# Kernel tuning notes

Measured on AMD Instinct MI355X. Metric: run time of the kernel, lower is better.

Reference implementation:

```python
import jax, jax.numpy as jnp
import numpy as np

EPS = 1e-5
NUM_HEADS = 12

def layer_norm(x, g, b):
    mu = jnp.mean(x, axis=-1, keepdims=True)
    var = jnp.var(x, axis=-1, keepdims=True)
    return (x - mu) * jax.lax.rsqrt(var + EPS) * g + b

def setup_inputs() -> dict:
    key = jax.random.key(0)
    ks = jax.random.split(key, 8)
    B, N, Dv, Ds, F = 8, 1024, 768, 512, 768
    def w(k, shape, fan_in):
        return jax.random.normal(k, shape, jnp.float32) * (fan_in ** -0.5)
    return dict(
        visual_features=jax.random.normal(ks[0], (B, N, Dv), jnp.float32),
        semantic_features=jax.random.normal(ks[1], (B, Ds), jnp.float32),
        Wq=w(ks[2], (F, Ds), Ds),
        Wk=w(ks[3], (F, Dv), Dv),
        Wv=w(ks[4], (F, Dv), Dv),
        Wo=w(ks[5], (Dv, F), F),
        bo=jnp.zeros((Dv,), jnp.float32),
        Wg=w(ks[6], (Dv, Dv + Ds), Dv + Ds),
        bg=jnp.zeros((Dv,), jnp.float32),
        gv=jnp.ones((Dv,), jnp.float32),
        bv=jnp.zeros((Dv,), jnp.float32),
        gs=jnp.ones((Ds,), jnp.float32),
        bs=jnp.zeros((Ds,), jnp.float32),
    )

def reference(visual_features, semantic_features, Wq, Wk, Wv, Wo, bo, Wg, bg, gv, bv, gs, bs):
    B, N, Dv = visual_features.shape
    F = Wq.shape[0]
    H = NUM_HEADS
    dh = F // H
    scale = dh ** -0.5
    vis_n = layer_norm(visual_features, gv, bv)           # (B,N,Dv)
    sem_n = layer_norm(semantic_features, gs, bs)         # (B,Ds) — LN over last dim; broadcast-invariant
    # Query is identical for every patch row -> exact single-query collapse of the N x N attention
    q = (sem_n @ Wq.T).reshape(B, H, dh)                  # (B,H,dh)
    k = (vis_n @ Wk.T).reshape(B, N, H, dh).transpose(0, 2, 1, 3)  # (B,H,N,dh)
    v = (vis_n @ Wv.T).reshape(B, N, H, dh).transpose(0, 2, 1, 3)  # (B,H,N,dh)
    scores = jnp.einsum('bhd,bhnd->bhn', q, k) * scale
    attn = jax.nn.softmax(scores, axis=-1)
    ctx = jnp.einsum('bhn,bhnd->bhd', attn, v).reshape(B, F)
    attended = ctx @ Wo.T + bo                            # (B,Dv), same for all N rows (dropout in eval = identity)
    sem_b = jnp.broadcast_to(semantic_features[:, None, :], (B, N, semantic_features.shape[-1]))
    gate_in = jnp.concatenate([visual_features, sem_b], axis=-1)   # (B,N,Dv+Ds)
    gate = jax.nn.sigmoid(gate_in @ Wg.T + bg)            # (B,N,Dv)
    return visual_features + gate * attended[:, None, :]
```

## Files before the change

kernel.cpp:

```cpp
#include <hip/hip_runtime.h>
#include <hip/hip_bf16.h>
#include <math.h>


typedef __attribute__((ext_vector_type(8))) short bf16x8;
typedef __attribute__((ext_vector_type(4))) float f32x4;

#define LN_EPS 1e-5f

__device__ __forceinline__ float bf2f(__hip_bfloat16 h){ return __bfloat162float(h); }

union bfpk8 { uint4 u; __hip_bfloat16 h[8]; };
union bfpk4 { uint2 u; __hip_bfloat16 h[4]; };

__device__ __align__(16) __hip_bfloat16 c_x[8*1024*768];
__device__ __align__(16) __hip_bfloat16 c_sem[8*512];
__device__ __align__(16) __hip_bfloat16 c_Wq[768*512];
__device__ __align__(16) __hip_bfloat16 c_Wk[768*768];
__device__ __align__(16) __hip_bfloat16 c_Wv[768*768];
__device__ __align__(16) __hip_bfloat16 c_Wo[768*768];
__device__ __align__(16) __hip_bfloat16 c_bo[768];
__device__ __align__(16) __hip_bfloat16 c_Wg[768*1280];
__device__ __align__(16) __hip_bfloat16 c_bg[768];
__device__ __align__(16) __hip_bfloat16 c_gv[768];
__device__ __align__(16) __hip_bfloat16 c_bv[768];
__device__ __align__(16) __hip_bfloat16 c_gs[512];
__device__ __align__(16) __hip_bfloat16 c_bs[512];

__device__ __align__(16) __hip_bfloat16 g_gqb[8*16*768];
__device__ __align__(16) float g_A[8*12*768];
__device__ __align__(16) float g_sgq[96];
__device__ __align__(16) float g_bq[96];
__device__ __align__(16) float g_mu[8192];
__device__ __align__(16) float g_rstd[8192];
__device__ __align__(16) float g_w[8*12*1024];
__device__ __align__(16) float g_C[96];
__device__ __align__(16) float g_ctx[8*768];
__device__ __align__(16) float g_att[8*768];

__device__ __forceinline__ int detect_bf16(const void* gv_raw){
    return ((const unsigned int*)gv_raw)[0] == 0x3F803F80u;
}

__device__ __forceinline__ void conv8(const void* __restrict__ src,
                                      __hip_bfloat16* __restrict__ dst,
                                      int g, int isb){
    if(isb){
        ((uint4*)dst)[g] = ((const uint4*)src)[g];
    } else {
        const float* s = (const float*)src + (size_t)g*8;
        bfpk8 o;
        #pragma unroll
        for(int e=0;e<8;e++) o.h[e] = __float2bfloat16(s[e]);
        ((uint4*)dst)[g] = o.u;
    }
}

#define ING_BLKS 1925
__global__ void k_ingest(const void* s1, const void* s2, const void* s3,
                         const void* s4, const void* s5, const void* s6, const void* s7,
                         const void* s8, const void* s9, const void* s10, const void* s11,
                         const void* s12){
    int i = blockIdx.x*256 + threadIdx.x;
    int isb = detect_bf16(s9);
    if     (i <    512) conv8(s1, c_sem, i,         isb);
    else if(i <  49664) conv8(s2, c_Wq,  i-   512,  isb);
    else if(i < 123392) conv8(s3, c_Wk,  i- 49664,  isb);
    else if(i < 197120) conv8(s4, c_Wv,  i-123392,  isb);
    else if(i < 270848) conv8(s5, c_Wo,  i-197120,  isb);
    else if(i < 270944) conv8(s6, c_bo,  i-270848,  isb);
    else if(i < 393824) conv8(s7, c_Wg,  i-270944,  isb);
    else if(i < 393920) conv8(s8, c_bg,  i-393824,  isb);
    else if(i < 394016) conv8(s9, c_gv,  i-393920,  isb);
    else if(i < 394112) conv8(s10,c_bv,  i-394016,  isb);
    else if(i < 394176) conv8(s11,c_gs,  i-394112,  isb);
    else if(i < 394240) conv8(s12,c_bs,  i-394176,  isb);
    else if(i < 467968) g_A[i-394240]   = 0.f;
    else if(i < 468064) g_sgq[i-467968] = 0.f;
    else if(i < 468160) g_bq[i-468064]  = 0.f;
    else if(i < 474304) g_ctx[i-468160] = 0.f;
    else if(i < 480448) g_att[i-474304] = 0.f;
    else if(i < 492736){
        uint4 z; z.x=0; z.y=0; z.z=0; z.w=0;
        ((uint4*)g_gqb)[i-480448] = z;
    }
}

__global__ void k_qhead(){
    __shared__ float s_semn[8*512];
    __shared__ float s_q2[8][64];
    __shared__ float s_sgq[8], s_bq[8];
    const int t = threadIdx.x, h = blockIdx.y;
    {
        int b = t>>5, l = t&31;
        bfpk8 p0, p1;
        p0.u = *(const uint4*)(c_sem + b*512 + l*16);
        p1.u = *(const uint4*)(c_sem + b*512 + l*16 + 8);
        float v[16], s = 0.f, s2 = 0.f;
        #pragma unroll
        for(int e=0;e<8;e++){ v[e]   = bf2f(p0.h[e]); s += v[e];   s2 += v[e]*v[e]; }
        #pragma unroll
        for(int e=0;e<8;e++){ v[8+e] = bf2f(p1.h[e]); s += v[8+e]; s2 += v[8+e]*v[8+e]; }
        #pragma unroll
        for(int o=16;o>0;o>>=1){ s += __shfl_xor(s,o); s2 += __shfl_xor(s2,o); }
        float mu = s*(1.f/512.f);
        float rstd = rsqrtf(s2*(1.f/512.f) - mu*mu + LN_EPS);
        bfpk8 g0, g1, b0, b1;
        g0.u = *(const uint4*)(c_gs + l*16);   g1.u = *(const uint4*)(c_gs + l*16 + 8);
        b0.u = *(const uint4*)(c_bs + l*16);   b1.u = *(const uint4*)(c_bs + l*16 + 8);
        #pragma unroll
        for(int e=0;e<8;e++){
            s_semn[b*512 + l*16 + e]     = (v[e]-mu)*rstd*bf2f(g0.h[e]) + bf2f(b0.h[e]);
            s_semn[b*512 + l*16 + 8 + e] = (v[8+e]-mu)*rstd*bf2f(g1.h[e]) + bf2f(b1.h[e]);
        }
    }
    if(t < 8){ s_sgq[t] = 0.f; s_bq[t] = 0.f; }
    __syncthreads();
    {
        int fi = t & 63, bp = t >> 6;
        int f = h*64 + fi;
        const __hip_bfloat16* wr = c_Wq + (size_t)f*512;
        float a0 = 0.f, a1 = 0.f;
        for(int i0=0;i0<512;i0+=8){
            bfpk8 pk; pk.u = *(const uint4*)(wr + i0);
            #pragma unroll
            for(int c=0;c<8;c++){
                float wv = bf2f(pk.h[c]);
                a0 += wv*s_semn[bp*512 + i0 + c];
                a1 += wv*s_semn[(bp+4)*512 + i0 + c];
            }
        }
        s_q2[bp][fi] = a0; s_q2[bp+4][fi] = a1;
    }
    __syncthreads();
    int dv = blockIdx.x*256 + t;
    float acc[8] = {0,0,0,0,0,0,0,0};
    for(int j=0;j<64;j++){
        float wk = bf2f(c_Wk[(size_t)(h*64+j)*768 + dv]);
        #pragma unroll
        for(int b=0;b<8;b++) acc[b] += s_q2[b][j]*wk;
    }
    float gvv = bf2f(c_gv[dv]), bvv = bf2f(c_bv[dv]);
    #pragma unroll
    for(int b=0;b<8;b++){
        float g = acc[b]*gvv;
        g_gqb[((size_t)b*16+h)*768 + dv] = __float2bfloat16(g);
        float sg = g, sb = bvv*acc[b];
        #pragma unroll
        for(int o=32;o>0;o>>=1){ sg += __shfl_xor(sg,o); sb += __shfl_xor(sb,o); }
        if((t&63)==0){ atomicAdd(&s_sgq[b], sg); atomicAdd(&s_bq[b], sb); }
    }
    __syncthreads();
    if(t < 8){ atomicAdd(&g_sgq[t*12+h], s_sgq[t]); atomicAdd(&g_bq[t*12+h], s_bq[t]); }
}

__global__ __launch_bounds__(64)
void k_scores(const void* __restrict__ xraw, const void* __restrict__ gvraw){
    __shared__ float s_mu[16], s_rstd[16];
    const int b = blockIdx.y;
    const int lane = threadIdx.x;
    const int isb = detect_bf16(gvraw);
    const int fr = lane & 15, quad = lane >> 4;
    const int n_tile = blockIdx.x*16;
    const size_t row = (size_t)b*1024 + n_tile + fr;
    const __hip_bfloat16* Bp = g_gqb + (size_t)b*16*768 + (size_t)fr*768;

    f32x4 acc = {};
    float s = 0.f, s2 = 0.f;
    if(isb){
        const __hip_bfloat16* xr = (const __hip_bfloat16*)xraw + row*768;
        for(int kb=0; kb<768; kb+=32){
            bfpk8 pk; pk.u = *(const uint4*)(xr + kb + quad*8);
            *(uint4*)(c_x + row*768 + kb + quad*8) = pk.u;
            #pragma unroll
            for(int e=0;e<8;e++){ float f = bf2f(pk.h[e]); s += f; s2 += f*f; }
            bf16x8 bfrag = *(const bf16x8*)(Bp + kb + quad*8);
            acc = __builtin_amdgcn_mfma_f32_16x16x32_bf16(*(const bf16x8*)&pk, bfrag, acc, 0,0,0);
        }
    } else {
        const float* xr = (const float*)xraw + row*768;
        for(int kb=0; kb<768; kb+=32){
            f32x4 x0 = *(const f32x4*)(xr + kb + quad*8);
            f32x4 x1 = *(const f32x4*)(xr + kb + quad*8 + 4);
            bfpk8 pk;
            #pragma unroll
            for(int e=0;e<4;e++){ pk.h[e]   = __float2bfloat16(x0[e]); s += x0[e]; s2 += x0[e]*x0[e]; }
            #pragma unroll
            for(int e=0;e<4;e++){ pk.h[4+e] = __float2bfloat16(x1[e]); s += x1[e]; s2 += x1[e]*x1[e]; }
            *(uint4*)(c_x + row*768 + kb + quad*8) = pk.u;
            bf16x8 bfrag = *(const bf16x8*)(Bp + kb + quad*8);
            acc = __builtin_amdgcn_mfma_f32_16x16x32_bf16(*(const bf16x8*)&pk, bfrag, acc, 0,0,0);
        }
    }
    s  += __shfl_xor(s, 16);  s  += __shfl_xor(s, 32);
    s2 += __shfl_xor(s2, 16); s2 += __shfl_xor(s2, 32);
    float mu = s*(1.f/768.f);
    float rstd = rsqrtf(s2*(1.f/768.f) - mu*mu + LN_EPS);
    if(quad == 0){
        g_mu[b*1024 + n_tile + fr] = mu;
        g_rstd[b*1024 + n_tile + fr] = rstd;
        s_mu[fr] = mu; s_rstd[fr] = rstd;
    }
    __syncthreads();
    if(fr < 12){
        float sgqh = g_sgq[b*12+fr];
        float bqh  = g_bq [b*12+fr];
        #pragma unroll
        for(int r=0;r<4;r++){
            int rr = quad*4 + r;
            float val = 0.125f*( s_rstd[rr]*(acc[r] - s_mu[rr]*sgqh) + bqh );
            g_w[((size_t)b*12+fr)*1024 + n_tile + rr] = val;
        }
    }
}

__global__ void k_softmax(){
    int bh = blockIdx.x, b = bh/12, t = threadIdx.x;
    float* sc = g_w + (size_t)bh*1024;
    f32x4 v = *(f32x4*)(sc + t*4);
    float m = fmaxf(fmaxf(v[0],v[1]), fmaxf(v[2],v[3]));
    __shared__ float redm[4], reds[4], redc[4];
    #pragma unroll
    for(int o=32;o>0;o>>=1) m = fmaxf(m, __shfl_xor(m,o));
    if((t&63)==0) redm[t>>6] = m;
    __syncthreads();
    m = fmaxf(fmaxf(redm[0],redm[1]), fmaxf(redm[2],redm[3]));
    float e0=expf(v[0]-m), e1=expf(v[1]-m), e2=expf(v[2]-m), e3=expf(v[3]-m);
    float s = e0+e1+e2+e3;
    #pragma unroll
    for(int o=32;o>0;o>>=1) s += __shfl_xor(s,o);
    if((t&63)==0) reds[t>>6] = s;
    __syncthreads();
    s = reds[0]+reds[1]+reds[2]+reds[3];
    float inv = 1.f/s;
    f32x4 rv = *(f32x4*)(g_rstd + b*1024 + t*4);
    f32x4 mv = *(f32x4*)(g_mu   + b*1024 + t*4);
    f32x4 o4;
    o4[0]=e0*inv*rv[0]; o4[1]=e1*inv*rv[1]; o4[2]=e2*inv*rv[2]; o4[3]=e3*inv*rv[3];
    *(f32x4*)(sc + t*4) = o4;
    float cp = o4[0]*mv[0] + o4[1]*mv[1] + o4[2]*mv[2] + o4[3]*mv[3];
    #pragma unroll
    for(int o=32;o>0;o>>=1) cp += __shfl_xor(cp,o);
    if((t&63)==0) redc[t>>6] = cp;
    __syncthreads();
    if(t==0) g_C[bh] = redc[0]+redc[1]+redc[2]+redc[3];
}

__global__ void k_accA(){
    __shared__ float s_w[12*128];
    int t = threadIdx.x, b = blockIdx.z, n0 = blockIdx.y*128;
    for(int i=t;i<12*128;i+=256){
        int h = i>>7, n = i&127;
        s_w[i] = g_w[((size_t)b*12+h)*1024 + n0 + n];
    }
    __syncthreads();
    int dv = blockIdx.x*256 + t;
    float acc[12] = {0,0,0,0,0,0,0,0,0,0,0,0};
    for(int n=0;n<128;n++){
        float xv = bf2f(c_x[(size_t)(b*1024+n0+n)*768 + dv]);
        #pragma unroll
        for(int h=0;h<12;h++) acc[h] += s_w[h*128+n]*xv;
    }
    #pragma unroll
    for(int h=0;h<12;h++) atomicAdd(&g_A[((size_t)b*12+h)*768 + dv], acc[h]);
}

__global__ void k_ctx(){
    __shared__ float s_wvis[8*260];
    int h = blockIdx.x, ch = blockIdx.y, t = threadIdx.x;
    int base = ch*256;
    for(int i=t;i<8*256;i+=512){
        int b = i>>8, dvl = i&255;
        int dv = base + dvl;
        s_wvis[b*260+dvl] = bf2f(c_gv[dv])*(g_A[((size_t)b*12+h)*768+dv] - g_C[b*12+h]) + bf2f(c_bv[dv]);
    }
    __syncthreads();
    int f = h*64 + (t>>3), b = t&7;
    const __hip_bfloat16* wr = c_Wv + (size_t)f*768 + base;
    float acc = 0.f;
    for(int d0=0;d0<256;d0+=8){
        bfpk8 pk; pk.u = *(const uint4*)(wr + d0);
        #pragma unroll
        for(int c=0;c<8;c++) acc += s_wvis[b*260 + d0 + c]*bf2f(pk.h[c]);
    }
    atomicAdd(&g_ctx[b*768+f], acc);
}

__global__ void k_att(){
    __shared__ float s_ctx[8*260];
    int ch = blockIdx.y, t = threadIdx.x;
    int base = ch*256;
    for(int i=t;i<8*256;i+=512){
        int b = i>>8, fl = i&255;
        s_ctx[b*260+fl] = g_ctx[b*768 + base + fl];
    }
    __syncthreads();
    int dv2 = blockIdx.x*64 + (t>>3), b = t&7;
    const __hip_bfloat16* wr = c_Wo + (size_t)dv2*768 + base;
    float acc = (ch==0) ? bf2f(c_bo[dv2]) : 0.f;
    for(int f0=0;f0<256;f0+=8){
        bfpk8 pk; pk.u = *(const uint4*)(wr + f0);
        #pragma unroll
        for(int c=0;c<8;c++) acc += s_ctx[b*260 + f0 + c]*bf2f(pk.h[c]);
    }
    atomicAdd(&g_att[b*768+dv2], acc);
}

__device__ __forceinline__ void stage_gate(int buf, int kb, int m0, int n0, int b_blk,
                                           __hip_bfloat16* As, __hip_bfloat16* Bs,
                                           int wave, int lane){
    const int rl = lane >> 2;
    const int kc = (lane & 3)*8;
    #pragma unroll
    for(int s=0;s<2;s++){
        int c = wave + 4*s;
        int row = c*16 + rl;
        const __hip_bfloat16* gp = (kb < 768)
            ? c_x + (size_t)(m0+row)*768 + kb + kc
            : c_sem + b_blk*512 + (kb-768) + kc;
        __builtin_amdgcn_global_load_lds(
            (const __attribute__((address_space(1))) void*)gp,
            (__attribute__((address_space(3))) void*)(As + buf*4096 + c*512),
            16, 0, 0);
    }
    {
        int c = wave;
        int row = c*16 + rl;
        const __hip_bfloat16* gp = c_Wg + (size_t)(n0+row)*1280 + kb + kc;
        __builtin_amdgcn_global_load_lds(
            (const __attribute__((address_space(1))) void*)gp,
            (__attribute__((address_space(3))) void*)(Bs + buf*2048 + c*512),
            16, 0, 0);
    }
}

__global__ __launch_bounds__(256)
void k_gate(void* __restrict__ outv, const void* __restrict__ gv_raw){
    __shared__ __align__(16) __hip_bfloat16 As[2*128*32];
    __shared__ __align__(16) __hip_bfloat16 Bs[2*64*32];
    const int isb = detect_bf16(gv_raw);
    const int t = threadIdx.x;
    const int n0 = blockIdx.x*64;
    const int m0 = blockIdx.y*128;
    const int b_blk = m0 >> 10;
    const int lane = t & 63, wave = t >> 6;
    const int wm = (wave>>1)*64, wn = (wave&1)*32;
    const int fr = lane & 15, quad = lane >> 4;

    f32x4 acc[4][2] = {};

    stage_gate(0, 0, m0, n0, b_blk, As, Bs, wave, lane);
    for(int it=0; it<40; it++){
        __syncthreads();
        if(it+1 < 40)
            stage_gate((it+1)&1, (it+1)*32, m0, n0, b_blk, As, Bs, wave, lane);
        const __hip_bfloat16* Ab = As + (it&1)*4096;
        const __hip_bfloat16* Bb = Bs + (it&1)*2048;
        bf16x8 af[4], bfr[2];
        #pragma unroll
        for(int i=0;i<4;i++) af[i]  = *(const bf16x8*)(Ab + (wm + i*16 + fr)*32 + quad*8);
        #pragma unroll
        for(int j=0;j<2;j++) bfr[j] = *(const bf16x8*)(Bb + (wn + j*16 + fr)*32 + quad*8);
        #pragma unroll
        for(int i=0;i<4;i++)
            #pragma unroll
            for(int j=0;j<2;j++)
                acc[i][j] = __builtin_amdgcn_mfma_f32_16x16x32_bf16(af[i], bfr[j], acc[i][j], 0,0,0);
    }

    #pragma unroll
    for(int j=0;j<2;j++){
        int col = n0 + wn + j*16 + fr;
        float attv = g_att[b_blk*768 + col];
        float bgv  = bf2f(c_bg[col]);
        #pragma unroll
        for(int i=0;i<4;i++){
            int mbase = m0 + wm + i*16 + quad*4;
            #pragma unroll
            for(int r=0;r<4;r++){
                int m = mbase + r;
                float g = acc[i][j][r] + bgv;
                g = fminf(fmaxf(g, -60.f), 60.f);
                float gate = 1.f/(1.f + expf(-g));
                float xv = bf2f(c_x[(size_t)m*768 + col]);
                float val = xv + gate*attv;
                size_t idx = (size_t)m*768 + col;
                if(isb) ((__hip_bfloat16*)outv)[idx] = __float2bfloat16(val);
                else    ((float*)outv)[idx] = val;
            }
        }
    }
}

extern "C" void kernel_launch(void* const* d_in, const int* in_sizes, int n_in,
                              void* d_out, int out_size, void* d_ws, size_t ws_size,
                              hipStream_t stream){
    (void)in_sizes; (void)n_in; (void)out_size; (void)d_ws; (void)ws_size;

    k_ingest<<<dim3(ING_BLKS), dim3(256), 0, stream>>>(d_in[1], d_in[2], d_in[3],
                                                       d_in[4], d_in[5], d_in[6], d_in[7],
                                                       d_in[8], d_in[9], d_in[10], d_in[11],
                                                       d_in[12]);
    k_qhead<<<dim3(3,12), dim3(256), 0, stream>>>();
    k_scores<<<dim3(64,8), dim3(64), 0, stream>>>(d_in[0], d_in[9]);
    k_softmax<<<dim3(96), dim3(256), 0, stream>>>();
    k_accA<<<dim3(3,8,8), dim3(256), 0, stream>>>();
    k_ctx<<<dim3(12,3), dim3(512), 0, stream>>>();
    k_att<<<dim3(12,3), dim3(512), 0, stream>>>();
    k_gate<<<dim3(12,64), dim3(256), 0, stream>>>(d_out, d_in[9]);
}
```

Before: 230.9 us.

## Precompute semantic gate term, split-K scores, swizzle LDS and remap gate blocks

The semantic part of the gate GEMM is constant across all N rows of a batch, so it is now computed once per batch in a new small kernel and added as a bias, which shrinks the gate GEMM K from 1280 to 768. The scores kernel now uses four waves per block, each handling a quarter of K, and combines partial MFMA results and LN statistics through shared memory. The gate kernel gains an XOR swizzle on its LDS staging to reduce bank conflicts, plus a block-index remap meant to improve cache locality. These changes add one extra kernel launch and extra shared-memory reductions.

Measured after the change: 210.0 us. 9.1% less time.

```diff
diff --git a/kernel.cpp b/kernel.cpp
--- a/kernel.cpp
+++ b/kernel.cpp
@@ -37,6 +37,7 @@
 __device__ __align__(16) float g_C[96];
 __device__ __align__(16) float g_ctx[8*768];
 __device__ __align__(16) float g_att[8*768];
+__device__ __align__(16) float g_gsem[8*768];
 
 __device__ __forceinline__ int detect_bf16(const void* gv_raw){
     return ((const unsigned int*)gv_raw)[0] == 0x3F803F80u;
@@ -154,22 +155,57 @@
     if(t < 8){ atomicAdd(&g_sgq[t*12+h], s_sgq[t]); atomicAdd(&g_bq[t*12+h], s_bq[t]); }
 }
 
-__global__ __launch_bounds__(64)
+__global__ __launch_bounds__(256)
+void k_gsem(){
+    __shared__ float s_sem[8*512];
+    __shared__ __hip_bfloat16 s_wg[16*520];
+    __shared__ float s_part[128];
+    const int t = threadIdx.x;
+    const int col0 = blockIdx.x*16;
+    for(int i=t;i<512;i+=256){
+        bfpk8 p; p.u = *(const uint4*)(c_sem + i*8);
+        #pragma unroll
+        for(int e=0;e<8;e++) s_sem[i*8+e] = bf2f(p.h[e]);
+    }
+    for(int i=t;i<16*64;i+=256){
+        int rl = i>>6, c = i&63;
+        *(uint4*)(s_wg + rl*520 + c*8) =
+            *(const uint4*)(c_Wg + (size_t)(col0+rl)*1280 + 768 + c*8);
+    }
+    __syncthreads();
+    const int cl = t&15, bh = t>>4, bb = bh&7, half = bh>>3;
+    const __hip_bfloat16* wr = s_wg + cl*520 + half*256;
+    const float* sr = s_sem + bb*512 + half*256;
+    float a = 0.f;
+    for(int k=0;k<256;k+=8){
+        bfpk8 p; p.u = *(const uint4*)(wr + k);
+        #pragma unroll
+        for(int e=0;e<8;e++) a += bf2f(p.h[e])*sr[k+e];
+    }
+    if(half) s_part[t&127] = a;
+    __syncthreads();
+    if(!half) g_gsem[bb*768 + col0 + cl] = a + s_part[t&127];
+}
+
+__global__ __launch_bounds__(256)
 void k_scores(const void* __restrict__ xraw, const void* __restrict__ gvraw){
+    __shared__ float s_acc[256*4];
+    __shared__ float s_s[4][16], s_s2[4][16];
     __shared__ float s_mu[16], s_rstd[16];
     const int b = blockIdx.y;
-    const int lane = threadIdx.x;
+    const int t = threadIdx.x, lane = t & 63, w = t >> 6;
     const int isb = detect_bf16(gvraw);
     const int fr = lane & 15, quad = lane >> 4;
     const int n_tile = blockIdx.x*16;
     const size_t row = (size_t)b*1024 + n_tile + fr;
     const __hip_bfloat16* Bp = g_gqb + (size_t)b*16*768 + (size_t)fr*768;
+    const int k0 = w*192;
 
     f32x4 acc = {};
     float s = 0.f, s2 = 0.f;
     if(isb){
         const __hip_bfloat16* xr = (const __hip_bfloat16*)xraw + row*768;
-        for(int kb=0; kb<768; kb+=32){
+        for(int kb=k0; kb<k0+192; kb+=32){
             bfpk8 pk; pk.u = *(const uint4*)(xr + kb + quad*8);
             *(uint4*)(c_x + row*768 + kb + quad*8) = pk.u;
             #pragma unroll
@@ -179,7 +215,7 @@
         }
     } else {
         const float* xr = (const float*)xraw + row*768;
-        for(int kb=0; kb<768; kb+=32){
+        for(int kb=k0; kb<k0+192; kb+=32){
             f32x4 x0 = *(const f32x4*)(xr + kb + quad*8);
             f32x4 x1 = *(const f32x4*)(xr + kb + quad*8 + 4);
             bfpk8 pk;
@@ -194,15 +230,27 @@
     }
     s  += __shfl_xor(s, 16);  s  += __shfl_xor(s, 32);
     s2 += __shfl_xor(s2, 16); s2 += __shfl_xor(s2, 32);
-    float mu = s*(1.f/768.f);
-    float rstd = rsqrtf(s2*(1.f/768.f) - mu*mu + LN_EPS);
-    if(quad == 0){
-        g_mu[b*1024 + n_tile + fr] = mu;
-        g_rstd[b*1024 + n_tile + fr] = rstd;
-        s_mu[fr] = mu; s_rstd[fr] = rstd;
-    }
-    __syncthreads();
-    if(fr < 12){
+    *(f32x4*)&s_acc[t*4] = acc;
+    if(quad == 0){ s_s[w][fr] = s; s_s2[w][fr] = s2; }
+    __syncthreads();
+    if(w == 0){
+        #pragma unroll
+        for(int ww=1;ww<4;ww++){
+            f32x4 o = *(const f32x4*)&s_acc[(ww*64+lane)*4];
+            acc[0]+=o[0]; acc[1]+=o[1]; acc[2]+=o[2]; acc[3]+=o[3];
+        }
+        if(quad == 0){
+            float st  = s_s[0][fr]+s_s[1][fr]+s_s[2][fr]+s_s[3][fr];
+            float st2 = s_s2[0][fr]+s_s2[1][fr]+s_s2[2][fr]+s_s2[3][fr];
+            float mu = st*(1.f/768.f);
+            float rstd = rsqrtf(st2*(1.f/768.f) - mu*mu + LN_EPS);
+            g_mu[b*1024 + n_tile + fr] = mu;
+            g_rstd[b*1024 + n_tile + fr] = rstd;
+            s_mu[fr] = mu; s_rstd[fr] = rstd;
+        }
+    }
+    __syncthreads();
+    if(w == 0 && fr < 12){
         float sgqh = g_sgq[b*12+fr];
         float bqh  = g_bq [b*12+fr];
         #pragma unroll
@@ -306,18 +354,16 @@
     atomicAdd(&g_att[b*768+dv2], acc);
 }
 
-__device__ __forceinline__ void stage_gate(int buf, int kb, int m0, int n0, int b_blk,
+__device__ __forceinline__ void stage_gate(int buf, int kb, int m0, int n0,
                                            __hip_bfloat16* As, __hip_bfloat16* Bs,
                                            int wave, int lane){
     const int rl = lane >> 2;
-    const int kc = (lane & 3)*8;
+    const int kc = ((lane & 3) ^ ((rl >> 1) & 3))*8;
     #pragma unroll
     for(int s=0;s<2;s++){
         int c = wave + 4*s;
         int row = c*16 + rl;
-        const __hip_bfloat16* gp = (kb < 768)
-            ? c_x + (size_t)(m0+row)*768 + kb + kc
-            : c_sem + b_blk*512 + (kb-768) + kc;
+        const __hip_bfloat16* gp = c_x + (size_t)(m0+row)*768 + kb + kc;
         __builtin_amdgcn_global_load_lds(
             (const __attribute__((address_space(1))) void*)gp,
             (__attribute__((address_space(3))) void*)(As + buf*4096 + c*512),
@@ -340,27 +386,30 @@
     __shared__ __align__(16) __hip_bfloat16 Bs[2*64*32];
     const int isb = detect_bf16(gv_raw);
     const int t = threadIdx.x;
-    const int n0 = blockIdx.x*64;
-    const int m0 = blockIdx.y*128;
+    const int lin  = blockIdx.y*12 + blockIdx.x;
+    const int wgid = (lin & 7)*96 + (lin >> 3);
+    const int n0 = (wgid % 12)*64;
+    const int m0 = (wgid / 12)*128;
     const int b_blk = m0 >> 10;
     const int lane = t & 63, wave = t >> 6;
     const int wm = (wave>>1)*64, wn = (wave&1)*32;
     const int fr = lane & 15, quad = lane >> 4;
+    const int sq = (quad ^ ((fr >> 1) & 3))*8;
 
     f32x4 acc[4][2] = {};
 
-    stage_gate(0, 0, m0, n0, b_blk, As, Bs, wave, lane);
-    for(int it=0; it<40; it++){
+    stage_gate(0, 0, m0, n0, As, Bs, wave, lane);
+    for(int it=0; it<24; it++){
         __syncthreads();
-        if(it+1 < 40)
-            stage_gate((it+1)&1, (it+1)*32, m0, n0, b_blk, As, Bs, wave, lane);
+        if(it+1 < 24)
+            stage_gate((it+1)&1, (it+1)*32, m0, n0, As, Bs, wave, lane);
         const __hip_bfloat16* Ab = As + (it&1)*4096;
         const __hip_bfloat16* Bb = Bs + (it&1)*2048;
         bf16x8 af[4], bfr[2];
         #pragma unroll
-        for(int i=0;i<4;i++) af[i]  = *(const bf16x8*)(Ab + (wm + i*16 + fr)*32 + quad*8);
-        #pragma unroll
-        for(int j=0;j<2;j++) bfr[j] = *(const bf16x8*)(Bb + (wn + j*16 + fr)*32 + quad*8);
+        for(int i=0;i<4;i++) af[i]  = *(const bf16x8*)(Ab + (wm + i*16 + fr)*32 + sq);
+        #pragma unroll
+        for(int j=0;j<2;j++) bfr[j] = *(const bf16x8*)(Bb + (wn + j*16 + fr)*32 + sq);
         #pragma unroll
         for(int i=0;i<4;i++)
             #pragma unroll
@@ -372,7 +421,7 @@
     for(int j=0;j<2;j++){
         int col = n0 + wn + j*16 + fr;
         float attv = g_att[b_blk*768 + col];
-        float bgv  = bf2f(c_bg[col]);
+        float bgv  = bf2f(c_bg[col]) + g_gsem[b_blk*768 + col];
         #pragma unroll
         for(int i=0;i<4;i++){
             int mbase = m0 + wm + i*16 + quad*4;
@@ -402,7 +451,8 @@
                                                        d_in[8], d_in[9], d_in[10], d_in[11],
                                                        d_in[12]);
     k_qhead<<<dim3(3,12), dim3(256), 0, stream>>>();
-    k_scores<<<dim3(64,8), dim3(64), 0, stream>>>(d_in[0], d_in[9]);
+    k_gsem<<<dim3(48), dim3(256), 0, stream>>>();
+    k_scores<<<dim3(64,8), dim3(256), 0, stream>>>(d_in[0], d_in[9]);
     k_softmax<<<dim3(96), dim3(256), 0, stream>>>();
     k_accA<<<dim3(3,8,8), dim3(256), 0, stream>>>();
     k_ctx<<<dim3(12,3), dim3(512), 0, stream>>>();
```
